# Performance work log

Measured on AMD Instinct MI355X. Metric: run time of the kernel, lower is better.

Reference implementation:

```python
import jax, jax.numpy as jnp
import numpy as np

D = 1024      # embed_dim
E = 2048      # expand * embed_dim
S_DIM = 128   # shrunken attn dim s
C = 256       # chunk size
SRC = 4096    # src_len
G = SRC // C  # num chunks
B = 8
STD = 0.02


def setup_inputs() -> dict:
    key = jax.random.key(0)
    ks = jax.random.split(key, 16)
    n = lambda k, shp: jax.random.normal(k, shp, dtype=jnp.float32)
    inp = {
        "query": n(ks[0], (SRC, B, D)),
        "key":   n(ks[1], (SRC, B, D)),
        "value": n(ks[2], (SRC, B, D)),
        # learned params (torch Linear stored as [in, out])
        "Wxs": n(ks[3], (D, S_DIM)) * STD, "bxs": n(ks[4], (S_DIM,)) * STD,
        "Wve": n(ks[5], (D, E)) * STD,     "bve": n(ks[6], (E,)) * STD,
        "Wue": n(ks[7], (D, E)) * STD,     "bue": n(ks[8], (E,)) * STD,
        "Wod": n(ks[9], (E, D)) * STD,     "bod": n(ks[10], (D,)) * STD,
        "rel_bias": n(ks[11], (C,)) * STD,
        "gamma": n(ks[12], (4, S_DIM)) * STD,
        "beta":  n(ks[13], (4, S_DIM)) * STD,
    }
    return inp


def reference(query, key, value, Wxs, bxs, Wve, bve, Wue, bue, Wod, bod,
              rel_bias, gamma, beta):
    # [S, B, D] -> [B, G, C, D]
    x = jnp.transpose(value, (1, 0, 2)).reshape(B, G, C, D)
    v = jnp.tanh(x @ Wve + bve)          # [b,g,c,e]
    z = jnp.tanh(x @ Wxs + bxs)          # [b,g,c,s]
    q_quad = z * gamma[0] + beta[0]
    k_quad = z * gamma[1] + beta[1]
    q_lin  = z * gamma[2] + beta[2]
    k_lin  = z * gamma[3] + beta[3]
    # local quadratic attention: relu(qk + bias)^2
    qk = jnp.einsum('bgns,bgms->bgnm', q_quad, k_quad)
    a = jnp.square(jax.nn.relu(qk + rel_bias))
    v_quad = jnp.einsum('bgnm,bgme->bgne', a, v)
    # global linear attention
    kv = jnp.einsum('bgcs,bgce->bse', k_lin, v)
    v_lin = jnp.einsum('bgcs,bse->bgce', q_lin, kv)
    u = jnp.tanh(x @ Wue + bue)          # [b,g,c,e]
    o = (u * (v_quad + v_lin)) @ Wod + bod   # [b,g,c,d]
    o = o.reshape(B, G * C, D)
    return jnp.transpose(o, (1, 0, 2))   # [S, B, D]
```

## Files before the change

kernel.cpp:

```cpp
#include <hip/hip_runtime.h>
#include <hip/hip_bf16.h>

using u16 = unsigned short;
using u32 = unsigned int;

typedef __attribute__((ext_vector_type(8))) short bf8;
typedef __attribute__((ext_vector_type(4))) float f4;
typedef __attribute__((ext_vector_type(4))) u16  us4;

#define DEV static __device__ __forceinline__

DEV float bf2f(u16 u) { return __uint_as_float(((u32)u) << 16); }
DEV u16 f2bf(float f) {
    u32 x = __float_as_uint(f);
    x += 0x7FFFu + ((x >> 16) & 1u);
    return (u16)(x >> 16);
}
DEV float tanhf_fast(float x) {
    float e = __expf(2.0f * x);
    return 1.0f - 2.0f / (e + 1.0f);
}
DEV f4 MFMA(bf8 a, bf8 b, f4 c) {
    return __builtin_amdgcn_mfma_f32_16x16x32_bf16(a, b, c, 0, 0, 0);
}
DEV int xcd_swz(int bx, int nwg) { return (bx & 7) * (nwg >> 3) + (bx >> 3); }


#define WS_XB    ((size_t)0)
#define WS_WXST  ((size_t)67108864)
#define WS_WVET  ((size_t)67371008)
#define WS_WUET  ((size_t)71565312)
#define WS_WODT  ((size_t)75759616)
#define WS_KVT   ((size_t)79953920)
#define WS_A     ((size_t)84148224)
#define WS_QL    ((size_t)100925440)
#define WS_VT    ((size_t)109314048)
#define WS_T1    ((size_t)243531776)
#define WS_Z     ((size_t)243531776)
#define WS_KLT   ((size_t)251920384)
#define WS_QQ    ((size_t)260308992)
#define WS_KQ    ((size_t)268697600)
#define WS_KVF   ((size_t)277086208)


DEV void stage128x64(const u16* __restrict__ gbase, int ld, u16* lds, int w, int lane) {
    const int srow = lane >> 3;
    const int scol = ((lane & 7) ^ srow) * 8;
    #pragma unroll
    for (int i = 0; i < 4; i++) {
        const int rt = (i * 4 + w) * 8 + srow;
        const u16* src = gbase + (size_t)rt * ld + scol;
        u16* dst = lds + (size_t)(i * 4 + w) * 512;
        __builtin_amdgcn_global_load_lds(
            (const __attribute__((address_space(1))) void*)src,
            (__attribute__((address_space(3))) void*)dst, 16, 0, 0);
    }
}

DEV void frag_mfma_64_swz(const u16* As, const u16* Bs, int wm, int wn, int ln, int lh,
                          f4 acc[4][4]) {
    #pragma unroll
    for (int kk2 = 0; kk2 < 2; kk2++) {
        const int sx = (((kk2 << 2) + lh) ^ (ln & 7)) << 3;
        bf8 a[4], b[4];
        #pragma unroll
        for (int mt = 0; mt < 4; mt++)
            a[mt] = *reinterpret_cast<const bf8*>(As + (wm * 64 + mt * 16 + ln) * 64 + sx);
        #pragma unroll
        for (int nt = 0; nt < 4; nt++)
            b[nt] = *reinterpret_cast<const bf8*>(Bs + (wn * 64 + nt * 16 + ln) * 64 + sx);
        #pragma unroll
        for (int mt = 0; mt < 4; mt++)
            #pragma unroll
            for (int nt = 0; nt < 4; nt++)
                acc[mt][nt] = MFMA(a[mt], b[nt], acc[mt][nt]);
    }
}

template<int NT, typename FA, typename FB>
DEV void gemm_pipe(FA stageA, FB stageB, u16* As, u16* Bs,
                   int wm, int wn, int ln, int lh, f4 acc[4][4]) {
    stageA(As, 0); stageB(Bs, 0);
    #pragma unroll 2
    for (int t = 0; t + 1 < NT; ++t) {
        u16* An = As + ((t & 1) ^ 1) * 8192;
        u16* Bn = Bs + ((t & 1) ^ 1) * 8192;
        stageA(An, t + 1); stageB(Bn, t + 1);
        asm volatile("s_waitcnt vmcnt(8)" ::: "memory");
        __builtin_amdgcn_s_barrier();
        __builtin_amdgcn_sched_barrier(0);
        frag_mfma_64_swz(As + (t & 1) * 8192, Bs + (t & 1) * 8192, wm, wn, ln, lh, acc);
        __builtin_amdgcn_sched_barrier(0);
        __builtin_amdgcn_s_barrier();
        __builtin_amdgcn_sched_barrier(0);
    }
    asm volatile("s_waitcnt vmcnt(0)" ::: "memory");
    __builtin_amdgcn_s_barrier();
    frag_mfma_64_swz(As + ((NT - 1) & 1) * 8192, Bs + ((NT - 1) & 1) * 8192, wm, wn, ln, lh, acc);
    __builtin_amdgcn_s_barrier();
}

__global__ void k_cvt_x(const float* __restrict__ src, u16* __restrict__ dst) {
    int m = blockIdx.x;
    int s = m >> 3, b = m & 7;
    const float* in = src + (size_t)m * 1024;
    u16* outp = dst + (((size_t)b << 12) + s) * 1024;
    int t = threadIdx.x * 4;
    float4 v = *reinterpret_cast<const float4*>(in + t);
    us4 o; o[0] = f2bf(v.x); o[1] = f2bf(v.y); o[2] = f2bf(v.z); o[3] = f2bf(v.w);
    *reinterpret_cast<us4*>(outp + t) = o;
}

__global__ void k_transpose(const float* __restrict__ src, u16* __restrict__ dst, int R, int C) {
    __shared__ u16 tile[32][33];
    int tx = threadIdx.x & 31, ty = threadIdx.x >> 5;
    int r0 = blockIdx.y * 32, c0 = blockIdx.x * 32;
    #pragma unroll
    for (int rr = ty; rr < 32; rr += 8)
        tile[rr][tx] = f2bf(src[(size_t)(r0 + rr) * C + c0 + tx]);
    __syncthreads();
    #pragma unroll
    for (int cc = ty; cc < 32; cc += 8)
        dst[(size_t)(c0 + cc) * R + r0 + tx] = tile[tx][cc];
}

__global__ void k_klinT(const u16* __restrict__ z, const float* __restrict__ gamma,
                        const float* __restrict__ beta, u16* __restrict__ klt) {
    __shared__ u16 tile[32][33];
    int tx = threadIdx.x & 31, ty = threadIdx.x >> 5;
    int r0 = blockIdx.x * 32;
    int c0 = blockIdx.y * 32;
    float gs = gamma[384 + c0 + tx], bs = beta[384 + c0 + tx];
    #pragma unroll
    for (int rr = ty; rr < 32; rr += 8) {
        u16 zv = z[(size_t)(r0 + rr) * 128 + c0 + tx];
        tile[rr][tx] = f2bf(bf2f(zv) * gs + bs);
    }
    __syncthreads();
    int b = r0 >> 12;
    int pos0 = r0 & 4095;
    #pragma unroll
    for (int cc = ty; cc < 32; cc += 8)
        klt[(((size_t)b * 128 + c0 + cc) << 12) + pos0 + tx] = tile[tx][cc];
}

__global__ __launch_bounds__(256) void k_zgemm(const u16* __restrict__ xb, const u16* __restrict__ WxsT,
                                               const float* __restrict__ bxs,
                                               const float* __restrict__ gamma, const float* __restrict__ beta,
                                               u16* __restrict__ z, u16* __restrict__ qq,
                                               u16* __restrict__ kq, u16* __restrict__ ql) {
    __shared__ u16 As[2][128 * 64];
    __shared__ u16 Bs[2][128 * 64];
    const int tid = threadIdx.x;
    const int lane = tid & 63, w = tid >> 6;
    const int ln = lane & 15, lh = lane >> 4;
    const int wm = w >> 1, wn = w & 1;
    const int rowbase = xcd_swz(blockIdx.x, 256) * 128;
    const u16* Ab = xb + (size_t)rowbase * 1024;
    f4 acc[4][4] = {};
    gemm_pipe<16>(
        [&](u16* l, int t) { stage128x64(Ab + t * 64, 1024, l, w, lane); },
        [&](u16* l, int t) { stage128x64(WxsT + t * 64, 1024, l, w, lane); },
        As[0], Bs[0], wm, wn, ln, lh, acc);
    #pragma unroll
    for (int mt = 0; mt < 4; mt++)
        #pragma unroll
        for (int nt = 0; nt < 4; nt++) {
            int col = wn * 64 + nt * 16 + ln;
            float bias = bxs[col];
            float g0 = gamma[col],       b0 = beta[col];
            float g1 = gamma[128 + col], b1 = beta[128 + col];
            float g2 = gamma[256 + col], b2 = beta[256 + col];
            int r0 = rowbase + wm * 64 + mt * 16 + lh * 4;
            #pragma unroll
            for (int rg = 0; rg < 4; rg++) {
                float zv = tanhf_fast(acc[mt][nt][rg] + bias);
                size_t idx = ((size_t)(r0 + rg) << 7) + col;
                z[idx]  = f2bf(zv);
                qq[idx] = f2bf(zv * g0 + b0);
                kq[idx] = f2bf(zv * g1 + b1);
                ql[idx] = f2bf(zv * g2 + b2);
            }
        }
}

__global__ __launch_bounds__(256) void k_vgemm(const u16* __restrict__ xb, const u16* __restrict__ WveT,
                                               const float* __restrict__ bve, u16* __restrict__ vT) {
    __shared__ u16 As[2][128 * 64];
    __shared__ u16 Bs[2][128 * 64];
    const int tid = threadIdx.x;
    const int lane = tid & 63, w = tid >> 6;
    const int ln = lane & 15, lh = lane >> 4;
    const int wm = w >> 1, wn = w & 1;
    const int rowbase = xcd_swz(blockIdx.x, 256) * 128;
    const int colbase = blockIdx.y * 128;
    const u16* Ab = xb + (size_t)rowbase * 1024;
    const u16* Bb = WveT + (size_t)colbase * 1024;
    f4 acc[4][4] = {};
    gemm_pipe<16>(
        [&](u16* l, int t) { stage128x64(Ab + t * 64, 1024, l, w, lane); },
        [&](u16* l, int t) { stage128x64(Bb + t * 64, 1024, l, w, lane); },
        As[0], Bs[0], wm, wn, ln, lh, acc);
    #pragma unroll
    for (int mt = 0; mt < 4; mt++)
        #pragma unroll
        for (int nt = 0; nt < 4; nt++) {
            int e = colbase + wn * 64 + nt * 16 + ln;
            float bias = bve[e];
            int r0 = rowbase + wm * 64 + mt * 16 + lh * 4;
            int bb = r0 >> 12, s0 = r0 & 4095;
            us4 p;
            #pragma unroll
            for (int rg = 0; rg < 4; rg++) p[rg] = f2bf(tanhf_fast(acc[mt][nt][rg] + bias));
            *reinterpret_cast<us4*>(vT + (((size_t)bb * 2048 + e) << 12) + s0) = p;
        }
}

__global__ __launch_bounds__(256) void k_kv(const u16* __restrict__ vT, const u16* __restrict__ klt,
                                            float* __restrict__ kvF) {
    __shared__ u16 As[2][128 * 64];
    __shared__ u16 Bs[2][128 * 64];
    const int tid = threadIdx.x;
    const int lane = tid & 63, w = tid >> 6;
    const int ln = lane & 15, lh = lane >> 4;
    const int wm = w >> 1, wn = w & 1;
    const int b = blockIdx.z;
    const int rowbase = blockIdx.x * 128;
    const int kbase = blockIdx.y * 1024;
    const u16* Ab = vT + ((size_t)b * 2048 + rowbase) * 4096 + kbase;
    const u16* Bb = klt + ((size_t)b * 128) * 4096 + kbase;
    f4 acc[4][4] = {};
    gemm_pipe<16>(
        [&](u16* l, int t) { stage128x64(Ab + t * 64, 4096, l, w, lane); },
        [&](u16* l, int t) { stage128x64(Bb + t * 64, 4096, l, w, lane); },
        As[0], Bs[0], wm, wn, ln, lh, acc);
    #pragma unroll
    for (int mt = 0; mt < 4; mt++)
        #pragma unroll
        for (int nt = 0; nt < 4; nt++) {
            int s = wn * 64 + nt * 16 + ln;
            int e0 = rowbase + wm * 64 + mt * 16 + lh * 4;
            #pragma unroll
            for (int rg = 0; rg < 4; rg++)
                atomicAdd(&kvF[(((size_t)b * 2048 + e0 + rg) << 7) + s], acc[mt][nt][rg]);
        }
}

__global__ void k_kvcvt(const float* __restrict__ kvF, u16* __restrict__ kvT, int n) {
    int i = (blockIdx.x * blockDim.x + threadIdx.x) * 4;
    if (i < n) {
        float4 v = *reinterpret_cast<const float4*>(kvF + i);
        us4 o; o[0] = f2bf(v.x); o[1] = f2bf(v.y); o[2] = f2bf(v.z); o[3] = f2bf(v.w);
        *reinterpret_cast<us4*>(kvT + i) = o;
    }
}

__global__ __launch_bounds__(256) void k_a(const u16* __restrict__ qq, const u16* __restrict__ kq,
                                           const float* __restrict__ rel_bias, u16* __restrict__ a_out) {
    const int lane = threadIdx.x & 63, wid = threadIdx.x >> 6;
    const int ln = lane & 15, lh = lane >> 4;
    const int wm = wid >> 1, wn = wid & 1;
    const int ci = blockIdx.y;
    const int qbase = blockIdx.x * 128 + wm * 64;
    const int nbase = wn * 128;
    const int rowbase = ci << 8;
    f4 acc[4][8] = {};
    const u16* qr[4];
    #pragma unroll
    for (int mt = 0; mt < 4; mt++) qr[mt] = qq + ((size_t)(rowbase + qbase + mt * 16 + ln) << 7);
    const u16* kr[8];
    #pragma unroll
    for (int nt = 0; nt < 8; nt++) kr[nt] = kq + ((size_t)(rowbase + nbase + nt * 16 + ln) << 7);
    #pragma unroll
    for (int kk = 0; kk < 128; kk += 32) {
        int k0 = kk + lh * 8;
        bf8 aq[4], ak[8];
        #pragma unroll
        for (int mt = 0; mt < 4; mt++) aq[mt] = *reinterpret_cast<const bf8*>(qr[mt] + k0);
        #pragma unroll
        for (int nt = 0; nt < 8; nt++) ak[nt] = *reinterpret_cast<const bf8*>(kr[nt] + k0);
        #pragma unroll
        for (int mt = 0; mt < 4; mt++)
            #pragma unroll
            for (int nt = 0; nt < 8; nt++)
                acc[mt][nt] = MFMA(aq[mt], ak[nt], acc[mt][nt]);
    }
    #pragma unroll
    for (int nt = 0; nt < 8; nt++) {
        int key = nbase + nt * 16 + ln;
        float rb = rel_bias[key];
        #pragma unroll
        for (int mt = 0; mt < 4; mt++) {
            int r0 = qbase + mt * 16 + lh * 4;
            #pragma unroll
            for (int rg = 0; rg < 4; rg++) {
                float v = acc[mt][nt][rg] + rb;
                v = fmaxf(v, 0.0f); v = v * v;
                a_out[((size_t)ci << 16) + ((size_t)(r0 + rg) << 8) + key] = f2bf(v);
            }
        }
    }
}

__global__ __launch_bounds__(256) void k_t1(const u16* __restrict__ ql, const u16* __restrict__ a_in,
                                            const u16* __restrict__ vT, const u16* __restrict__ kvT,
                                            u16* __restrict__ t1) {
    __shared__ u16 As[2][128 * 64];
    __shared__ u16 Bs[2][128 * 64];
    const int tid = threadIdx.x;
    const int lane = tid & 63, w = tid >> 6;
    const int ln = lane & 15, lh = lane >> 4;
    const int wm = w >> 1, wn = w & 1;
    const int bx = xcd_swz(blockIdx.x, 256);
    const int rowbase = bx * 128;
    const int ebase = blockIdx.y * 128;
    const int ci = bx >> 1;
    const int b = ci >> 4, g = ci & 15;
    f4 acc[4][4] = {};
    {
        const u16* Ab = ql + (size_t)rowbase * 128;
        const u16* Bb = kvT + ((size_t)(b * 2048 + ebase)) * 128;
        gemm_pipe<2>(
            [&](u16* l, int t) { stage128x64(Ab + t * 64, 128, l, w, lane); },
            [&](u16* l, int t) { stage128x64(Bb + t * 64, 128, l, w, lane); },
            As[0], Bs[0], wm, wn, ln, lh, acc);
    }
    {
        const int lqbase = (bx & 1) * 128;
        const u16* Ab = a_in + ((size_t)ci << 16) + (size_t)lqbase * 256;
        const u16* Bb = vT + ((size_t)(b * 2048 + ebase)) * 4096 + (g << 8);
        gemm_pipe<4>(
            [&](u16* l, int t) { stage128x64(Ab + t * 64, 256, l, w, lane); },
            [&](u16* l, int t) { stage128x64(Bb + t * 64, 4096, l, w, lane); },
            As[0], Bs[0], wm, wn, ln, lh, acc);
    }
    #pragma unroll
    for (int mt = 0; mt < 4; mt++)
        #pragma unroll
        for (int nt = 0; nt < 4; nt++) {
            int e = ebase + wn * 64 + nt * 16 + ln;
            int r0 = rowbase + wm * 64 + mt * 16 + lh * 4;
            #pragma unroll
            for (int rg = 0; rg < 4; rg++)
                t1[((size_t)(r0 + rg) << 11) + e] = f2bf(acc[mt][nt][rg]);
        }
}

__global__ __launch_bounds__(256) void k_u(const u16* __restrict__ xb, const u16* __restrict__ WueT,
                                           const float* __restrict__ bue, u16* t1) {
    __shared__ u16 As[2][128 * 64];
    __shared__ u16 Bs[2][128 * 64];
    const int tid = threadIdx.x;
    const int lane = tid & 63, w = tid >> 6;
    const int ln = lane & 15, lh = lane >> 4;
    const int wm = w >> 1, wn = w & 1;
    const int rowbase = xcd_swz(blockIdx.x, 256) * 128;
    const int colbase = blockIdx.y * 128;
    const u16* Ab = xb + (size_t)rowbase * 1024;
    const u16* Bb = WueT + (size_t)colbase * 1024;
    f4 acc[4][4] = {};
    gemm_pipe<16>(
        [&](u16* l, int t) { stage128x64(Ab + t * 64, 1024, l, w, lane); },
        [&](u16* l, int t) { stage128x64(Bb + t * 64, 1024, l, w, lane); },
        As[0], Bs[0], wm, wn, ln, lh, acc);
    #pragma unroll
    for (int mt = 0; mt < 4; mt++)
        #pragma unroll
        for (int nt = 0; nt < 4; nt++) {
            int e = colbase + wn * 64 + nt * 16 + ln;
            float bias = bue[e];
            int r0 = rowbase + wm * 64 + mt * 16 + lh * 4;
            #pragma unroll
            for (int rg = 0; rg < 4; rg++) {
                size_t idx = ((size_t)(r0 + rg) << 11) + e;
                float t = bf2f(t1[idx]);
                float u = tanhf_fast(acc[mt][nt][rg] + bias);
                t1[idx] = f2bf(u * t);
            }
        }
}

__global__ __launch_bounds__(256) void k_o(const u16* __restrict__ t1, const u16* __restrict__ WodT,
                                           const float* __restrict__ bod, float* __restrict__ out) {
    __shared__ u16 As[2][128 * 64];
    __shared__ u16 Bs[2][128 * 64];
    const int tid = threadIdx.x;
    const int lane = tid & 63, w = tid >> 6;
    const int ln = lane & 15, lh = lane >> 4;
    const int wm = w >> 1, wn = w & 1;
    const int rowbase = xcd_swz(blockIdx.x, 256) * 128;
    const int colbase = blockIdx.y * 128;
    const u16* Ab = t1 + (size_t)rowbase * 2048;
    const u16* Bb = WodT + (size_t)colbase * 2048;
    f4 acc[4][4] = {};
    gemm_pipe<32>(
        [&](u16* l, int t) { stage128x64(Ab + t * 64, 2048, l, w, lane); },
        [&](u16* l, int t) { stage128x64(Bb + t * 64, 2048, l, w, lane); },
        As[0], Bs[0], wm, wn, ln, lh, acc);
    #pragma unroll
    for (int mt = 0; mt < 4; mt++)
        #pragma unroll
        for (int nt = 0; nt < 4; nt++) {
            int d = colbase + wn * 64 + nt * 16 + ln;
            float bias = bod[d];
            int r0 = rowbase + wm * 64 + mt * 16 + lh * 4;
            #pragma unroll
            for (int rg = 0; rg < 4; rg++) {
                int r = r0 + rg;
                int s = r & 4095, bb = r >> 12;
                out[((size_t)(s * 8 + bb) << 10) + d] = acc[mt][nt][rg] + bias;
            }
        }
}

extern "C" void kernel_launch(void* const* d_in, const int* in_sizes, int n_in,
                              void* d_out, int out_size, void* d_ws, size_t ws_size,
                              hipStream_t stream) {
    const float* value = (const float*)d_in[2];
    const float* Wxs = (const float*)d_in[3];  const float* bxs = (const float*)d_in[4];
    const float* Wve = (const float*)d_in[5];  const float* bve = (const float*)d_in[6];
    const float* Wue = (const float*)d_in[7];  const float* bue = (const float*)d_in[8];
    const float* Wod = (const float*)d_in[9];  const float* bod = (const float*)d_in[10];
    const float* rel_bias = (const float*)d_in[11];
    const float* gamma = (const float*)d_in[12];
    const float* beta  = (const float*)d_in[13];
    float* out = (float*)d_out;

    char* ws = (char*)d_ws;
    u16* xb   = (u16*)(ws + WS_XB);
    u16* WxsT = (u16*)(ws + WS_WXST);
    u16* WveT = (u16*)(ws + WS_WVET);
    u16* WueT = (u16*)(ws + WS_WUET);
    u16* WodT = (u16*)(ws + WS_WODT);
    u16* kvT  = (u16*)(ws + WS_KVT);
    u16* a    = (u16*)(ws + WS_A);
    u16* ql   = (u16*)(ws + WS_QL);
    u16* vT   = (u16*)(ws + WS_VT);
    u16* t1   = (u16*)(ws + WS_T1);
    u16* z    = (u16*)(ws + WS_Z);
    u16* klt  = (u16*)(ws + WS_KLT);
    u16* qq   = (u16*)(ws + WS_QQ);
    u16* kq   = (u16*)(ws + WS_KQ);
    float* kvF = (float*)(ws + WS_KVF);

    k_cvt_x<<<32768, 256, 0, stream>>>(value, xb);
    k_transpose<<<dim3(4, 32),  256, 0, stream>>>(Wxs, WxsT, 1024, 128);
    k_transpose<<<dim3(64, 32), 256, 0, stream>>>(Wve, WveT, 1024, 2048);
    k_transpose<<<dim3(64, 32), 256, 0, stream>>>(Wue, WueT, 1024, 2048);
    k_transpose<<<dim3(32, 64), 256, 0, stream>>>(Wod, WodT, 2048, 1024);
    k_zgemm<<<256, 256, 0, stream>>>(xb, WxsT, bxs, gamma, beta, z, qq, kq, ql);
    k_klinT<<<dim3(1024, 4), 256, 0, stream>>>(z, gamma, beta, klt);
    k_vgemm<<<dim3(256, 16), 256, 0, stream>>>(xb, WveT, bve, vT);
    hipMemsetAsync(kvF, 0, (size_t)8 * 2048 * 128 * 4, stream);
    k_kv<<<dim3(16, 4, 8), 256, 0, stream>>>(vT, klt, kvF);
    k_kvcvt<<<2048, 256, 0, stream>>>(kvF, kvT, 8 * 2048 * 128);
    k_a<<<dim3(2, 128), 256, 0, stream>>>(qq, kq, rel_bias, a);
    k_t1<<<dim3(256, 16), 256, 0, stream>>>(ql, a, vT, kvT, t1);
    k_u<<<dim3(256, 16), 256, 0, stream>>>(xb, WueT, bue, t1);
    k_o<<<dim3(256, 8), 256, 0, stream>>>(t1, WodT, bod, out);
}
```

Measured before the change: 856.3 us.

## Use 256x256 tiles with 8 waves for the large GEMM kernels

Replaces the 128x128 tile, 4-wave GEMM pipeline in the v, u, o and t1 kernels with a 256x256 tile, 512-thread pipeline in which each wave computes a 128x64 sub-tile. The goal is to raise arithmetic intensity and cut global and LDS traffic per MFMA. The t1 kernel now runs its linear-attention and quadratic-attention K loops as one fused 6-step pipeline. The larger per-thread accumulator raises register pressure and each block uses 128 KB of LDS. With fewer blocks, occupancy and tail effects may suffer.

New measurement: 768.8 us. -10.2%, faster.

```diff
diff --git a/kernel.cpp b/kernel.cpp
--- a/kernel.cpp
+++ b/kernel.cpp
@@ -24,6 +24,12 @@
     return __builtin_amdgcn_mfma_f32_16x16x32_bf16(a, b, c, 0, 0, 0);
 }
 DEV int xcd_swz(int bx, int nwg) { return (bx & 7) * (nwg >> 3) + (bx >> 3); }
+
+DEV void gload16(const u16* src, u16* dst) {
+    __builtin_amdgcn_global_load_lds(
+        (const __attribute__((address_space(1))) void*)src,
+        (__attribute__((address_space(3))) void*)dst, 16, 0, 0);
+}
 
 
 #define WS_XB    ((size_t)0)
@@ -42,7 +48,6 @@
 #define WS_KQ    ((size_t)268697600)
 #define WS_KVF   ((size_t)277086208)
 
-
 DEV void stage128x64(const u16* __restrict__ gbase, int ld, u16* lds, int w, int lane) {
     const int srow = lane >> 3;
     const int scol = ((lane & 7) ^ srow) * 8;
@@ -51,9 +56,7 @@
         const int rt = (i * 4 + w) * 8 + srow;
         const u16* src = gbase + (size_t)rt * ld + scol;
         u16* dst = lds + (size_t)(i * 4 + w) * 512;
-        __builtin_amdgcn_global_load_lds(
-            (const __attribute__((address_space(1))) void*)src,
-            (__attribute__((address_space(3))) void*)dst, 16, 0, 0);
+        gload16(src, dst);
     }
 }
 
@@ -100,6 +103,66 @@
     __builtin_amdgcn_s_barrier();
 }
 
+
+#define T256 16384
+
+DEV void stage256x64(const u16* __restrict__ gbase, int ld, u16* lds, int tid) {
+    const int slot = tid & 7;
+    #pragma unroll
+    for (int i = 0; i < 4; i++) {
+        const int row = i * 64 + (tid >> 3);
+        const u16* src = gbase + (size_t)row * ld + ((slot ^ (row & 7)) << 3);
+        u16* dst = lds + ((size_t)(i * 512 + (tid & ~63)) << 3);
+        gload16(src, dst);
+    }
+}
+
+DEV void tile_mfma256(const u16* As, const u16* Bs, int wm, int wn, int ln, int lh,
+                      f4 acc[8][4]) {
+    __builtin_amdgcn_s_setprio(1);
+    #pragma unroll
+    for (int p = 0; p < 4; p++) {
+        const int mg = p >> 1, ks = p & 1;
+        const int sx = (((ks << 2) + lh) ^ (ln & 7)) << 3;
+        bf8 a[4], b[4];
+        #pragma unroll
+        for (int j = 0; j < 4; j++)
+            a[j] = *reinterpret_cast<const bf8*>(As + (wm * 128 + (mg * 4 + j) * 16 + ln) * 64 + sx);
+        #pragma unroll
+        for (int n = 0; n < 4; n++)
+            b[n] = *reinterpret_cast<const bf8*>(Bs + (wn * 64 + n * 16 + ln) * 64 + sx);
+        #pragma unroll
+        for (int j = 0; j < 4; j++)
+            #pragma unroll
+            for (int n = 0; n < 4; n++)
+                acc[mg * 4 + j][n] = MFMA(a[j], b[n], acc[mg * 4 + j][n]);
+        __builtin_amdgcn_sched_barrier(0);
+    }
+    __builtin_amdgcn_s_setprio(0);
+}
+
+template<int NT, typename F>
+DEV void gemm_pipe256(F stage, u16* As, u16* Bs, int wm, int wn, int ln, int lh,
+                      f4 acc[8][4]) {
+    stage(As, Bs, 0);
+    #pragma unroll 2
+    for (int t = 0; t + 1 < NT; ++t) {
+        const int cur = t & 1, nxt = cur ^ 1;
+        stage(As + nxt * T256, Bs + nxt * T256, t + 1);
+        asm volatile("s_waitcnt vmcnt(8)" ::: "memory");
+        __builtin_amdgcn_s_barrier();
+        __builtin_amdgcn_sched_barrier(0);
+        tile_mfma256(As + cur * T256, Bs + cur * T256, wm, wn, ln, lh, acc);
+        __builtin_amdgcn_sched_barrier(0);
+        __builtin_amdgcn_s_barrier();
+        __builtin_amdgcn_sched_barrier(0);
+    }
+    asm volatile("s_waitcnt vmcnt(0)" ::: "memory");
+    __builtin_amdgcn_s_barrier();
+    tile_mfma256(As + ((NT - 1) & 1) * T256, Bs + ((NT - 1) & 1) * T256, wm, wn, ln, lh, acc);
+    __builtin_amdgcn_s_barrier();
+}
+
 __global__ void k_cvt_x(const float* __restrict__ src, u16* __restrict__ dst) {
     int m = blockIdx.x;
     int s = m >> 3, b = m & 7;
@@ -184,30 +247,32 @@
         }
 }
 
-__global__ __launch_bounds__(256) void k_vgemm(const u16* __restrict__ xb, const u16* __restrict__ WveT,
-                                               const float* __restrict__ bve, u16* __restrict__ vT) {
-    __shared__ u16 As[2][128 * 64];
-    __shared__ u16 Bs[2][128 * 64];
+__global__ __launch_bounds__(512, 2) void k_vgemm(const u16* __restrict__ xb, const u16* __restrict__ WveT,
+                                                  const float* __restrict__ bve, u16* __restrict__ vT) {
+    __shared__ u16 As[2 * T256];
+    __shared__ u16 Bs[2 * T256];
     const int tid = threadIdx.x;
     const int lane = tid & 63, w = tid >> 6;
     const int ln = lane & 15, lh = lane >> 4;
-    const int wm = w >> 1, wn = w & 1;
-    const int rowbase = xcd_swz(blockIdx.x, 256) * 128;
-    const int colbase = blockIdx.y * 128;
+    const int wm = w >> 2, wn = w & 3;
+    const int rowbase = xcd_swz(blockIdx.x, 128) * 256;
+    const int colbase = blockIdx.y * 256;
     const u16* Ab = xb + (size_t)rowbase * 1024;
     const u16* Bb = WveT + (size_t)colbase * 1024;
-    f4 acc[4][4] = {};
-    gemm_pipe<16>(
-        [&](u16* l, int t) { stage128x64(Ab + t * 64, 1024, l, w, lane); },
-        [&](u16* l, int t) { stage128x64(Bb + t * 64, 1024, l, w, lane); },
-        As[0], Bs[0], wm, wn, ln, lh, acc);
-    #pragma unroll
-    for (int mt = 0; mt < 4; mt++)
+    f4 acc[8][4] = {};
+    gemm_pipe256<16>(
+        [&](u16* a, u16* b, int t) {
+            stage256x64(Ab + t * 64, 1024, a, tid);
+            stage256x64(Bb + t * 64, 1024, b, tid);
+        },
+        As, Bs, wm, wn, ln, lh, acc);
+    #pragma unroll
+    for (int mt = 0; mt < 8; mt++)
         #pragma unroll
         for (int nt = 0; nt < 4; nt++) {
             int e = colbase + wn * 64 + nt * 16 + ln;
             float bias = bve[e];
-            int r0 = rowbase + wm * 64 + mt * 16 + lh * 4;
+            int r0 = rowbase + wm * 128 + mt * 16 + lh * 4;
             int bb = r0 >> 12, s0 = r0 & 4095;
             us4 p;
             #pragma unroll
@@ -302,74 +367,73 @@
     }
 }
 
-__global__ __launch_bounds__(256) void k_t1(const u16* __restrict__ ql, const u16* __restrict__ a_in,
-                                            const u16* __restrict__ vT, const u16* __restrict__ kvT,
-                                            u16* __restrict__ t1) {
-    __shared__ u16 As[2][128 * 64];
-    __shared__ u16 Bs[2][128 * 64];
+__global__ __launch_bounds__(512, 2) void k_t1(const u16* __restrict__ ql, const u16* __restrict__ a_in,
+                                               const u16* __restrict__ vT, const u16* __restrict__ kvT,
+                                               u16* __restrict__ t1) {
+    __shared__ u16 As[2 * T256];
+    __shared__ u16 Bs[2 * T256];
     const int tid = threadIdx.x;
     const int lane = tid & 63, w = tid >> 6;
     const int ln = lane & 15, lh = lane >> 4;
-    const int wm = w >> 1, wn = w & 1;
-    const int bx = xcd_swz(blockIdx.x, 256);
-    const int rowbase = bx * 128;
-    const int ebase = blockIdx.y * 128;
-    const int ci = bx >> 1;
+    const int wm = w >> 2, wn = w & 3;
+    const int ci = xcd_swz(blockIdx.x, 128);
+    const int rowbase = ci << 8;
+    const int ebase = blockIdx.y * 256;
     const int b = ci >> 4, g = ci & 15;
-    f4 acc[4][4] = {};
-    {
-        const u16* Ab = ql + (size_t)rowbase * 128;
-        const u16* Bb = kvT + ((size_t)(b * 2048 + ebase)) * 128;
-        gemm_pipe<2>(
-            [&](u16* l, int t) { stage128x64(Ab + t * 64, 128, l, w, lane); },
-            [&](u16* l, int t) { stage128x64(Bb + t * 64, 128, l, w, lane); },
-            As[0], Bs[0], wm, wn, ln, lh, acc);
-    }
-    {
-        const int lqbase = (bx & 1) * 128;
-        const u16* Ab = a_in + ((size_t)ci << 16) + (size_t)lqbase * 256;
-        const u16* Bb = vT + ((size_t)(b * 2048 + ebase)) * 4096 + (g << 8);
-        gemm_pipe<4>(
-            [&](u16* l, int t) { stage128x64(Ab + t * 64, 256, l, w, lane); },
-            [&](u16* l, int t) { stage128x64(Bb + t * 64, 4096, l, w, lane); },
-            As[0], Bs[0], wm, wn, ln, lh, acc);
-    }
-    #pragma unroll
-    for (int mt = 0; mt < 4; mt++)
+    const u16* Aa = ql + (size_t)rowbase * 128;
+    const u16* Ba = kvT + ((size_t)(b * 2048 + ebase)) * 128;
+    const u16* Ab = a_in + ((size_t)ci << 16);
+    const u16* Bb = vT + ((size_t)(b * 2048 + ebase)) * 4096 + (g << 8);
+    f4 acc[8][4] = {};
+    gemm_pipe256<6>(
+        [&](u16* a, u16* bl, int t) {
+            if (t < 2) {
+                stage256x64(Aa + t * 64, 128, a, tid);
+                stage256x64(Ba + t * 64, 128, bl, tid);
+            } else {
+                stage256x64(Ab + (t - 2) * 64, 256, a, tid);
+                stage256x64(Bb + (t - 2) * 64, 4096, bl, tid);
+            }
+        },
+        As, Bs, wm, wn, ln, lh, acc);
+    #pragma unroll
+    for (int mt = 0; mt < 8; mt++)
         #pragma unroll
         for (int nt = 0; nt < 4; nt++) {
             int e = ebase + wn * 64 + nt * 16 + ln;
-            int r0 = rowbase + wm * 64 + mt * 16 + lh * 4;
+            int r0 = rowbase + wm * 128 + mt * 16 + lh * 4;
             #pragma unroll
             for (int rg = 0; rg < 4; rg++)
                 t1[((size_t)(r0 + rg) << 11) + e] = f2bf(acc[mt][nt][rg]);
         }
 }
 
-__global__ __launch_bounds__(256) void k_u(const u16* __restrict__ xb, const u16* __restrict__ WueT,
-                                           const float* __restrict__ bue, u16* t1) {
-    __shared__ u16 As[2][128 * 64];
-    __shared__ u16 Bs[2][128 * 64];
+__global__ __launch_bounds__(512, 2) void k_u(const u16* __restrict__ xb, const u16* __restrict__ WueT,
+                                              const float* __restrict__ bue, u16* t1) {
+    __shared__ u16 As[2 * T256];
+    __shared__ u16 Bs[2 * T256];
     const int tid = threadIdx.x;
     const int lane = tid & 63, w = tid >> 6;
     const int ln = lane & 15, lh = lane >> 4;
-    const int wm = w >> 1, wn = w & 1;
-    const int rowbase = xcd_swz(blockIdx.x, 256) * 128;
-    const int colbase = blockIdx.y * 128;
+    const int wm = w >> 2, wn = w & 3;
+    const int rowbase = xcd_swz(blockIdx.x, 128) * 256;
+    const int colbase = blockIdx.y * 256;
     const u16* Ab = xb + (size_t)rowbase * 1024;
     const u16* Bb = WueT + (size_t)colbase * 1024;
-    f4 acc[4][4] = {};
-    gemm_pipe<16>(
-        [&](u16* l, int t) { stage128x64(Ab + t * 64, 1024, l, w, lane); },
-        [&](u16* l, int t) { stage128x64(Bb + t * 64, 1024, l, w, lane); },
-        As[0], Bs[0], wm, wn, ln, lh, acc);
-    #pragma unroll
-    for (int mt = 0; mt < 4; mt++)
+    f4 acc[8][4] = {};
+    gemm_pipe256<16>(
+        [&](u16* a, u16* b, int t) {
+            stage256x64(Ab + t * 64, 1024, a, tid);
+            stage256x64(Bb + t * 64, 1024, b, tid);
+        },
+        As, Bs, wm, wn, ln, lh, acc);
+    #pragma unroll
+    for (int mt = 0; mt < 8; mt++)
         #pragma unroll
         for (int nt = 0; nt < 4; nt++) {
             int e = colbase + wn * 64 + nt * 16 + ln;
             float bias = bue[e];
-            int r0 = rowbase + wm * 64 + mt * 16 + lh * 4;
+            int r0 = rowbase + wm * 128 + mt * 16 + lh * 4;
             #pragma unroll
             for (int rg = 0; rg < 4; rg++) {
                 size_t idx = ((size_t)(r0 + rg) << 11) + e;
@@ -380,30 +444,32 @@
         }
 }
 
-__global__ __launch_bounds__(256) void k_o(const u16* __restrict__ t1, const u16* __restrict__ WodT,
-                                           const float* __restrict__ bod, float* __restrict__ out) {
-    __shared__ u16 As[2][128 * 64];
-    __shared__ u16 Bs[2][128 * 64];
+__global__ __launch_bounds__(512, 2) void k_o(const u16* __restrict__ t1, const u16* __restrict__ WodT,
+                                              const float* __restrict__ bod, float* __restrict__ out) {
+    __shared__ u16 As[2 * T256];
+    __shared__ u16 Bs[2 * T256];
     const int tid = threadIdx.x;
     const int lane = tid & 63, w = tid >> 6;
     const int ln = lane & 15, lh = lane >> 4;
-    const int wm = w >> 1, wn = w & 1;
-    const int rowbase = xcd_swz(blockIdx.x, 256) * 128;
-    const int colbase = blockIdx.y * 128;
+    const int wm = w >> 2, wn = w & 3;
+    const int rowbase = xcd_swz(blockIdx.x, 128) * 256;
+    const int colbase = blockIdx.y * 256;
     const u16* Ab = t1 + (size_t)rowbase * 2048;
     const u16* Bb = WodT + (size_t)colbase * 2048;
-    f4 acc[4][4] = {};
-    gemm_pipe<32>(
-        [&](u16* l, int t) { stage128x64(Ab + t * 64, 2048, l, w, lane); },
-        [&](u16* l, int t) { stage128x64(Bb + t * 64, 2048, l, w, lane); },
-        As[0], Bs[0], wm, wn, ln, lh, acc);
-    #pragma unroll
-    for (int mt = 0; mt < 4; mt++)
+    f4 acc[8][4] = {};
+    gemm_pipe256<32>(
+        [&](u16* a, u16* b, int t) {
+            stage256x64(Ab + t * 64, 2048, a, tid);
+            stage256x64(Bb + t * 64, 2048, b, tid);
+        },
+        As, Bs, wm, wn, ln, lh, acc);
+    #pragma unroll
+    for (int mt = 0; mt < 8; mt++)
         #pragma unroll
         for (int nt = 0; nt < 4; nt++) {
             int d = colbase + wn * 64 + nt * 16 + ln;
             float bias = bod[d];
-            int r0 = rowbase + wm * 64 + mt * 16 + lh * 4;
+            int r0 = rowbase + wm * 128 + mt * 16 + lh * 4;
             #pragma unroll
             for (int rg = 0; rg < 4; rg++) {
                 int r = r0 + rg;
@@ -450,12 +516,12 @@
     k_transpose<<<dim3(32, 64), 256, 0, stream>>>(Wod, WodT, 2048, 1024);
     k_zgemm<<<256, 256, 0, stream>>>(xb, WxsT, bxs, gamma, beta, z, qq, kq, ql);
     k_klinT<<<dim3(1024, 4), 256, 0, stream>>>(z, gamma, beta, klt);
-    k_vgemm<<<dim3(256, 16), 256, 0, stream>>>(xb, WveT, bve, vT);
+    k_vgemm<<<dim3(128, 8), 512, 0, stream>>>(xb, WveT, bve, vT);
     hipMemsetAsync(kvF, 0, (size_t)8 * 2048 * 128 * 4, stream);
     k_kv<<<dim3(16, 4, 8), 256, 0, stream>>>(vT, klt, kvF);
     k_kvcvt<<<2048, 256, 0, stream>>>(kvF, kvT, 8 * 2048 * 128);
     k_a<<<dim3(2, 128), 256, 0, stream>>>(qq, kq, rel_bias, a);
-    k_t1<<<dim3(256, 16), 256, 0, stream>>>(ql, a, vT, kvT, t1);
-    k_u<<<dim3(256, 16), 256, 0, stream>>>(xb, WueT, bue, t1);
-    k_o<<<dim3(256, 8), 256, 0, stream>>>(t1, WodT, bod, out);
-}
+    k_t1<<<dim3(128, 8), 512, 0, stream>>>(ql, a, vT, kvT, t1);
+    k_u<<<dim3(128, 8), 512, 0, stream>>>(xb, WueT, bue, t1);
+    k_o<<<dim3(128, 4), 512, 0, stream>>>(t1, WodT, bod, out);
+}
```
